# Optimization experiments

Hardware: AMD Instinct MI355X
Metric: run time of the kernel (lower is better)

The kernel has to match this reference:

```python
import jax, jax.numpy as jnp
import numpy as np

N = 100_000   # nodes
E = 600_000   # edges
D = 128       # embed_dim
G = 1000      # graphs (batch ids)
L = 3         # num_layers


def setup_inputs() -> dict:
    key = jax.random.key(0)
    ks = jax.random.split(key, 12)
    s = 1.0 / np.sqrt(D)
    return {
        "x": jax.random.normal(ks[0], (N, D), jnp.float32),
        "edge_index": jax.random.randint(ks[1], (2, E), 0, N),
        "batch": jnp.sort(jax.random.randint(ks[2], (N,), 0, G)),
        "mask": jax.random.randint(ks[3], (N,), 0, 2),
        # stacked GCNConv weights/biases (in=hidden=out=D)
        "gcn_w": jax.random.normal(ks[4], (L, D, D), jnp.float32) * s,
        "gcn_b": jnp.zeros((L, D), jnp.float32),
        # MLP head: Linear(D,D) -> ReLU -> Linear(D,1)
        "lin1_w": jax.random.normal(ks[5], (D, D), jnp.float32) * s,
        "lin1_b": jnp.zeros((D,), jnp.float32),
        "lin2_w": jax.random.normal(ks[6], (D,), jnp.float32) * s,
        "lin2_b": jnp.zeros((), jnp.float32),
    }


def gcn_forward(x, src, dst, gcn_w, gcn_b):
    # symmetric gcn_norm with self-loops: deg[i] = 1 + in-degree(i)
    deg = jax.ops.segment_sum(jnp.ones((E,), x.dtype), dst, num_segments=N) + 1.0
    dinv = jax.lax.rsqrt(deg)
    enorm = dinv[src] * dinv[dst]          # [E] edge normalization
    self_norm = (dinv * dinv)[:, None]     # [N,1] self-loop normalization
    h = x
    for l in range(L):
        h = h @ gcn_w[l]                   # [N,D]
        h = (jax.ops.segment_sum(h[src] * enorm[:, None], dst, num_segments=N)
             + h * self_norm)
        h = h + gcn_b[l]
        if l < L - 1:
            h = jax.nn.relu(h)  # (dropout inactive at inference)
    return h


def reference(x, edge_index, batch, mask, gcn_w, gcn_b, lin1_w, lin1_b, lin2_w, lin2_b):
    src, dst = edge_index[0], edge_index[1]
    h = gcn_forward(x, src, dst, gcn_w, gcn_b)
    # MLP head -> per-node score [N]
    s = jax.nn.relu(h @ lin1_w + lin1_b) @ lin2_w + lin2_b
    s = jnp.where(mask == 0, jnp.float32(-1e9), s)
    # per-graph (segment) softmax — fused replacement for the unique/batch loop
    m = jax.ops.segment_max(s, batch, num_segments=G)
    e = jnp.exp(s - m[batch])
    z = jax.ops.segment_sum(e, batch, num_segments=G)
    return e / z[batch]
```

## Files before the change

### kernel.cpp

```cpp
#include <hip/hip_runtime.h>
#include <hip/hip_bf16.h>

typedef unsigned int u32;
typedef unsigned short u16;
typedef __attribute__((ext_vector_type(8))) short bf16x8;
typedef __attribute__((ext_vector_type(4))) float f32x4;

__device__ __forceinline__ float u16tof(u16 u){ return __uint_as_float(((u32)u) << 16); }
__device__ __forceinline__ float lo16(u32 v){ return __uint_as_float(v << 16); }
__device__ __forceinline__ float hi16(u32 v){ return __uint_as_float(v & 0xffff0000u); }
__device__ __forceinline__ u16 ftobf(float f){
  u32 b = __float_as_uint(f);
  return (u16)((b + 0x7FFFu + ((b >> 16) & 1u)) >> 16);
}
__device__ __forceinline__ u32 pack2(float a, float b){
  return (u32)ftobf(a) | ((u32)ftobf(b) << 16);
}
__device__ __forceinline__ float ldf(const void* p, int i, int isbf){
  return isbf ? u16tof(((const u16*)p)[i]) : ((const float*)p)[i];
}

__global__ __launch_bounds__(256) void k_prep(const void* __restrict__ gw, const void* __restrict__ l1w,
                                              const void* __restrict__ x, u16* __restrict__ Wf,
                                              u16* __restrict__ Hb, int L, int n8, int cvtB, int goffB,
                                              const int* __restrict__ batch, int* __restrict__ goff,
                                              int N, int G,
                                              const int* __restrict__ dst, int* __restrict__ hist,
                                              int nE, int chunk, int* __restrict__ flag){
  __shared__ int sh[256];
  const int b = blockIdx.x;
  const int t = threadIdx.x;
  const int histStart = L + 1 + cvtB + goffB;

  if (b >= histStart){
    sh[t] = 0; __syncthreads();
    const int blk = b - histStart;
    const int e0 = blk * chunk, e1 = min(e0 + chunk, nE);
    for (int e = e0 + t; e < e1; e += 256) atomicAdd(&sh[dst[e] >> 9], 1);
    __syncthreads();
    hist[blk * 256 + t] = sh[t];
    return;
  }
  if (b >= L + 1 + cvtB){
    const int i = (b - (L + 1 + cvtB)) * 256 + t;
    if (i >= N) return;
    const int bt = batch[i];
    const int prev = (i == 0) ? -1 : batch[i - 1];
    for (int g = prev + 1; g <= bt; ++g) goff[g] = i;
    if (i == N - 1){ for (int g = bt + 1; g <= G; ++g) goff[g] = N; }
    return;
  }
  if (t == 0) sh[0] = 0;
  __syncthreads();
  if (b <= L){
    int local = 0;
    for (int i = t; i < 4096; i += 256){
      u32 e = (((const u32*)gw)[i] >> 7) & 0xFFu;
      if (e >= 100u && e < 127u) local++;
    }
    atomicAdd(&sh[0], local);
    __syncthreads();
    const int isbf = (sh[0] > 2048) ? 1 : 0;
    if (b == 0 && t == 0) *flag = isbf;

    const void* src = (b < L) ? gw : l1w;
    const int sbase = (b < L) ? b * 16384 : 0;
    u16* dstp = Wf + (size_t)b * 16384;
    for (int g = t; g < 2048; g += 256){
      const int tt = g >> 8, ks = (g >> 6) & 3, lane = g & 63;
      const int n = tt * 16 + (lane & 15);
      const int k0 = ks * 32 + ((lane >> 4) << 3);
      u16* d = dstp + (size_t)g * 8;
      #pragma unroll
      for (int j = 0; j < 8; ++j){
        d[j] = ftobf(ldf(src, sbase + (k0 + j) * 128 + n, isbf));
      }
    }
  } else {
    u32 e = (((const u32*)gw)[t] >> 7) & 0xFFu;
    atomicAdd(&sh[0], (e >= 100u && e < 127u) ? 1 : 0);
    __syncthreads();
    if (sh[0] > 128) return;
    const int i = (b - (L + 1)) * 256 + t;
    if (i >= n8) return;
    const float4 a = ((const float4*)x)[i * 2];
    const float4 c = ((const float4*)x)[i * 2 + 1];
    u16* o = Hb + (size_t)i * 8;
    o[0] = ftobf(a.x); o[1] = ftobf(a.y); o[2] = ftobf(a.z); o[3] = ftobf(a.w);
    o[4] = ftobf(c.x); o[5] = ftobf(c.y); o[6] = ftobf(c.z); o[7] = ftobf(c.w);
  }
}

__global__ __launch_bounds__(256) void k_hscan(int* __restrict__ hist, int* __restrict__ bb, int nE){
  const int t = threadIdx.x;
  int run = 0;
  for (int j = 0; j < 256; ++j){
    const int v = hist[j * 256 + t];
    hist[j * 256 + t] = run;
    run += v;
  }
  __shared__ int sm[256];
  sm[t] = run; __syncthreads();
  for (int off = 1; off < 256; off <<= 1){
    int a = (t >= off) ? sm[t - off] : 0;
    __syncthreads();
    sm[t] += a;
    __syncthreads();
  }
  bb[t] = sm[t] - run;
  if (t == 255) bb[256] = nE;
}

__global__ __launch_bounds__(256) void k_scatter(const int* __restrict__ src, const int* __restrict__ dst,
                                                 const int* __restrict__ hist, const int* __restrict__ bb,
                                                 int2* __restrict__ tmpe, int nE, int chunk){
  __shared__ int base[256];
  const int blk = blockIdx.x, t = threadIdx.x;
  base[t] = bb[t] + hist[blk * 256 + t];
  __syncthreads();
  const int e0 = blk * chunk, e1 = min(e0 + chunk, nE);
  for (int e = e0 + t; e < e1; e += 256){
    const int d = dst[e];
    const int pos = atomicAdd(&base[d >> 9], 1);
    tmpe[pos] = make_int2(src[e], d);
  }
}

__global__ __launch_bounds__(256) void k_local(const int2* __restrict__ tmpe, const int* __restrict__ bb,
                                               int* __restrict__ boff, int* __restrict__ eid,
                                               float* __restrict__ dinv, int N, int nE, int nbkt){
  __shared__ int hcnt[512];
  __shared__ int hoff[512];
  const int b = blockIdx.x, t = threadIdx.x;
  const int n0 = b << 9;
  const int n1 = min(n0 + 512, N);
  const int nn = n1 - n0;
  const int e0 = bb[b], e1 = bb[b + 1];
  hcnt[t] = 0; hcnt[t + 256] = 0;
  __syncthreads();
  for (int e = e0 + t; e < e1; e += 256) atomicAdd(&hcnt[tmpe[e].y - n0], 1);
  __syncthreads();
  const int v0 = hcnt[t], v1 = hcnt[t + 256];
  hoff[t] = v0; hoff[t + 256] = v1;
  __syncthreads();
  for (int off = 1; off < 512; off <<= 1){
    int a0 = (t >= off) ? hoff[t - off] : 0;
    int a1 = (t + 256 >= off) ? hoff[t + 256 - off] : 0;
    __syncthreads();
    hoff[t] += a0; hoff[t + 256] += a1;
    __syncthreads();
  }
  const int ex0 = hoff[t] - v0 + e0;
  const int ex1 = hoff[t + 256] - v1 + e0;
  if (t < nn){       boff[n0 + t] = ex0;        dinv[n0 + t] = rsqrtf((float)v0 + 1.0f); }
  if (t + 256 < nn){ boff[n0 + t + 256] = ex1;  dinv[n0 + t + 256] = rsqrtf((float)v1 + 1.0f); }
  if (b == nbkt - 1 && t == 0) boff[N] = nE;
  __syncthreads();
  hoff[t] = ex0; hoff[t + 256] = ex1;
  __syncthreads();
  for (int e = e0 + t; e < e1; e += 256){
    const int2 pr = tmpe[e];
    const int pos = atomicAdd(&hoff[pr.y - n0], 1);
    eid[pos] = pr.x;
  }
}

__global__ __launch_bounds__(256) void k_mm(const void* __restrict__ X, const u16* __restrict__ Hb,
                                            const u16* __restrict__ Wf, const float* __restrict__ dinv,
                                            u16* __restrict__ T, int n, const int* __restrict__ fl){
  __shared__ u16 smw[16384];
  const int isbf = *fl;
  const u16* A = isbf ? (const u16*)X : Hb;
  {
    const uint4* s = (const uint4*)Wf;
    uint4* d = (uint4*)smw;
    for (int i = threadIdx.x; i < 2048; i += 256) d[i] = s[i];
  }
  __syncthreads();

  const int wave = threadIdx.x >> 6, lane = threadIdx.x & 63;
  const int m0 = blockIdx.x * 64 + wave * 16;
  int arow = m0 + (lane & 15); if (arow > n - 1) arow = n - 1;
  const u16* aptr = A + (size_t)arow * 128 + ((lane >> 4) << 3);

  f32x4 acc[8];
  #pragma unroll
  for (int t = 0; t < 8; ++t) acc[t] = (f32x4){0.f, 0.f, 0.f, 0.f};

  #pragma unroll
  for (int ks = 0; ks < 4; ++ks){
    const bf16x8 a = *(const bf16x8*)(aptr + ks * 32);
    #pragma unroll
    for (int t = 0; t < 8; ++t){
      const bf16x8 b = *(const bf16x8*)(smw + (size_t)(((t * 4 + ks) * 64 + lane) * 8));
      acc[t] = __builtin_amdgcn_mfma_f32_16x16x32_bf16(a, b, acc[t], 0, 0, 0);
    }
  }
  __syncthreads();

  const int quad = lane >> 4, col0 = lane & 15;
  float dv[4];
  #pragma unroll
  for (int r = 0; r < 4; ++r){
    const int row = m0 + quad * 4 + r;
    dv[r] = (row < n) ? dinv[row] : 0.f;
  }
  u16* my = smw + wave * 2112;
  #pragma unroll
  for (int t = 0; t < 8; ++t){
    #pragma unroll
    for (int r = 0; r < 4; ++r){
      my[(quad * 4 + r) * 132 + t * 16 + col0] = ftobf(acc[t][r] * dv[r]);
    }
  }
  #pragma unroll
  for (int i = 0; i < 4; ++i){
    const int row = i * 4 + (lane >> 4);
    const int grow = m0 + row;
    const int c8 = (lane & 15) * 8;
    if (grow < n){
      const u16* s = &my[row * 132 + c8];
      uint2 lo = *(const uint2*)(s);
      uint2 hi = *(const uint2*)(s + 4);
      *(uint4*)&T[(size_t)grow * 128 + c8] = make_uint4(lo.x, lo.y, hi.x, hi.y);
    }
  }
}

__global__ __launch_bounds__(256) void k_gmm(const u16* __restrict__ Tin, const int* __restrict__ boff,
                                             const int* __restrict__ eid, const float* __restrict__ dinv,
                                             const void* __restrict__ bias, int layer,
                                             const u16* __restrict__ Wf, u16* __restrict__ Tout,
                                             int n, const int* __restrict__ fl){
  __shared__ u16 sma[16 * 132];
  const int isbf = *fl;
  const int wave = threadIdx.x >> 6, lane = threadIdx.x & 63;
  const int sub = lane >> 4, l16 = lane & 15;
  const int m0 = blockIdx.x * 16;

  const int node = m0 + wave * 4 + sub;
  float h0=0,h1=0,h2=0,h3=0,h4=0,h5=0,h6=0,h7=0;
  if (node < n){
    const uint4 sv = ((const uint4*)(Tin + (size_t)node * 128))[l16];
    float a0 = lo16(sv.x), a1 = hi16(sv.x), a2 = lo16(sv.y), a3 = hi16(sv.y);
    float a4 = lo16(sv.z), a5 = hi16(sv.z), a6 = lo16(sv.w), a7 = hi16(sv.w);
    int j = boff[node];
    const int b1e = boff[node + 1];
    for (; j + 4 <= b1e; j += 4){
      const int s0 = eid[j], s1 = eid[j + 1], s2 = eid[j + 2], s3 = eid[j + 3];
      const uint4 v0 = ((const uint4*)(Tin + (size_t)s0 * 128))[l16];
      const uint4 v1 = ((const uint4*)(Tin + (size_t)s1 * 128))[l16];
      const uint4 v2 = ((const uint4*)(Tin + (size_t)s2 * 128))[l16];
      const uint4 v3 = ((const uint4*)(Tin + (size_t)s3 * 128))[l16];
      a0 += (lo16(v0.x) + lo16(v1.x)) + (lo16(v2.x) + lo16(v3.x));
      a1 += (hi16(v0.x) + hi16(v1.x)) + (hi16(v2.x) + hi16(v3.x));
      a2 += (lo16(v0.y) + lo16(v1.y)) + (lo16(v2.y) + lo16(v3.y));
      a3 += (hi16(v0.y) + hi16(v1.y)) + (hi16(v2.y) + hi16(v3.y));
      a4 += (lo16(v0.z) + lo16(v1.z)) + (lo16(v2.z) + lo16(v3.z));
      a5 += (hi16(v0.z) + hi16(v1.z)) + (hi16(v2.z) + hi16(v3.z));
      a6 += (lo16(v0.w) + lo16(v1.w)) + (lo16(v2.w) + lo16(v3.w));
      a7 += (hi16(v0.w) + hi16(v1.w)) + (hi16(v2.w) + hi16(v3.w));
    }
    for (; j < b1e; ++j){
      const uint4 v = ((const uint4*)(Tin + (size_t)eid[j] * 128))[l16];
      a0 += lo16(v.x); a1 += hi16(v.x);
      a2 += lo16(v.y); a3 += hi16(v.y);
      a4 += lo16(v.z); a5 += hi16(v.z);
      a6 += lo16(v.w); a7 += hi16(v.w);
    }
    const float di = dinv[node];
    const int bb = layer * 128 + l16 * 8;
    h0 = fmaxf(fmaf(a0, di, ldf(bias, bb + 0, isbf)), 0.f);
    h1 = fmaxf(fmaf(a1, di, ldf(bias, bb + 1, isbf)), 0.f);
    h2 = fmaxf(fmaf(a2, di, ldf(bias, bb + 2, isbf)), 0.f);
    h3 = fmaxf(fmaf(a3, di, ldf(bias, bb + 3, isbf)), 0.f);
    h4 = fmaxf(fmaf(a4, di, ldf(bias, bb + 4, isbf)), 0.f);
    h5 = fmaxf(fmaf(a5, di, ldf(bias, bb + 5, isbf)), 0.f);
    h6 = fmaxf(fmaf(a6, di, ldf(bias, bb + 6, isbf)), 0.f);
    h7 = fmaxf(fmaf(a7, di, ldf(bias, bb + 7, isbf)), 0.f);
  }
  {
    uint4 o;
    o.x = pack2(h0, h1); o.y = pack2(h2, h3); o.z = pack2(h4, h5); o.w = pack2(h6, h7);
    *(uint4*)&sma[(wave * 4 + sub) * 132 + l16 * 8] = o;
  }
  __syncthreads();

  f32x4 acc[2];
  acc[0] = (f32x4){0.f,0.f,0.f,0.f}; acc[1] = (f32x4){0.f,0.f,0.f,0.f};
  #pragma unroll
  for (int ks = 0; ks < 4; ++ks){
    const bf16x8 a = *(const bf16x8*)(sma + l16 * 132 + sub * 8 + ks * 32);
    #pragma unroll
    for (int tt = 0; tt < 2; ++tt){
      const int t = wave * 2 + tt;
      const bf16x8 b = *(const bf16x8*)(Wf + (size_t)(((t * 4 + ks) * 64 + lane) * 8));
      acc[tt] = __builtin_amdgcn_mfma_f32_16x16x32_bf16(a, b, acc[tt], 0, 0, 0);
    }
  }
  __syncthreads();

  float dv[4];
  #pragma unroll
  for (int r = 0; r < 4; ++r){
    const int row = m0 + sub * 4 + r;
    dv[r] = (row < n) ? dinv[row] : 0.f;
  }
  #pragma unroll
  for (int tt = 0; tt < 2; ++tt){
    const int t = wave * 2 + tt;
    #pragma unroll
    for (int r = 0; r < 4; ++r){
      sma[(sub * 4 + r) * 132 + t * 16 + l16] = ftobf(acc[tt][r] * dv[r]);
    }
  }
  __syncthreads();

  {
    const int row = threadIdx.x >> 4;
    const int c8 = (threadIdx.x & 15) * 8;
    if (m0 + row < n){
      const u16* s = &sma[row * 132 + c8];
      uint2 lo = *(const uint2*)(s);
      uint2 hi = *(const uint2*)(s + 4);
      *(uint4*)&Tout[(size_t)(m0 + row) * 128 + c8] = make_uint4(lo.x, lo.y, hi.x, hi.y);
    }
  }
}

__global__ __launch_bounds__(256) void k_ghead(const u16* __restrict__ Tin, const int* __restrict__ boff,
                                               const int* __restrict__ eid, const float* __restrict__ dinv,
                                               const void* __restrict__ bias, int layer,
                                               const u16* __restrict__ Wf, const void* __restrict__ b1,
                                               const void* __restrict__ w2, const void* __restrict__ b2,
                                               const int* __restrict__ mask, float* __restrict__ s,
                                               int n, const int* __restrict__ fl){
  __shared__ u16 sma[16 * 132];
  __shared__ float sred[4][16];
  const int isbf = *fl;
  const int wave = threadIdx.x >> 6, lane = threadIdx.x & 63;
  const int sub = lane >> 4, l16 = lane & 15;
  const int m0 = blockIdx.x * 16;

  const int node = m0 + wave * 4 + sub;
  float h0=0,h1=0,h2=0,h3=0,h4=0,h5=0,h6=0,h7=0;
  if (node < n){
    const uint4 sv = ((const uint4*)(Tin + (size_t)node * 128))[l16];
    float a0 = lo16(sv.x), a1 = hi16(sv.x), a2 = lo16(sv.y), a3 = hi16(sv.y);
    float a4 = lo16(sv.z), a5 = hi16(sv.z), a6 = lo16(sv.w), a7 = hi16(sv.w);
    int j = boff[node];
    const int b1e = boff[node + 1];
    for (; j + 4 <= b1e; j += 4){
      const int s0 = eid[j], s1 = eid[j + 1], s2 = eid[j + 2], s3 = eid[j + 3];
      const uint4 v0 = ((const uint4*)(Tin + (size_t)s0 * 128))[l16];
      const uint4 v1 = ((const uint4*)(Tin + (size_t)s1 * 128))[l16];
      const uint4 v2 = ((const uint4*)(Tin + (size_t)s2 * 128))[l16];
      const uint4 v3 = ((const uint4*)(Tin + (size_t)s3 * 128))[l16];
      a0 += (lo16(v0.x) + lo16(v1.x)) + (lo16(v2.x) + lo16(v3.x));
      a1 += (hi16(v0.x) + hi16(v1.x)) + (hi16(v2.x) + hi16(v3.x));
      a2 += (lo16(v0.y) + lo16(v1.y)) + (lo16(v2.y) + lo16(v3.y));
      a3 += (hi16(v0.y) + hi16(v1.y)) + (hi16(v2.y) + hi16(v3.y));
      a4 += (lo16(v0.z) + lo16(v1.z)) + (lo16(v2.z) + lo16(v3.z));
      a5 += (hi16(v0.z) + hi16(v1.z)) + (hi16(v2.z) + hi16(v3.z));
      a6 += (lo16(v0.w) + lo16(v1.w)) + (lo16(v2.w) + lo16(v3.w));
      a7 += (hi16(v0.w) + hi16(v1.w)) + (hi16(v2.w) + hi16(v3.w));
    }
    for (; j < b1e; ++j){
      const uint4 v = ((const uint4*)(Tin + (size_t)eid[j] * 128))[l16];
      a0 += lo16(v.x); a1 += hi16(v.x);
      a2 += lo16(v.y); a3 += hi16(v.y);
      a4 += lo16(v.z); a5 += hi16(v.z);
      a6 += lo16(v.w); a7 += hi16(v.w);
    }
    const float di = dinv[node];
    const int bb = layer * 128 + l16 * 8;
    h0 = fmaf(a0, di, ldf(bias, bb + 0, isbf));
    h1 = fmaf(a1, di, ldf(bias, bb + 1, isbf));
    h2 = fmaf(a2, di, ldf(bias, bb + 2, isbf));
    h3 = fmaf(a3, di, ldf(bias, bb + 3, isbf));
    h4 = fmaf(a4, di, ldf(bias, bb + 4, isbf));
    h5 = fmaf(a5, di, ldf(bias, bb + 5, isbf));
    h6 = fmaf(a6, di, ldf(bias, bb + 6, isbf));
    h7 = fmaf(a7, di, ldf(bias, bb + 7, isbf));
  }
  {
    uint4 o;
    o.x = pack2(h0, h1); o.y = pack2(h2, h3); o.z = pack2(h4, h5); o.w = pack2(h6, h7);
    *(uint4*)&sma[(wave * 4 + sub) * 132 + l16 * 8] = o;
  }
  __syncthreads();

  f32x4 acc[2];
  acc[0] = (f32x4){0.f,0.f,0.f,0.f}; acc[1] = (f32x4){0.f,0.f,0.f,0.f};
  #pragma unroll
  for (int ks = 0; ks < 4; ++ks){
    const bf16x8 a = *(const bf16x8*)(sma + l16 * 132 + sub * 8 + ks * 32);
    #pragma unroll
    for (int tt = 0; tt < 2; ++tt){
      const int t = wave * 2 + tt;
      const bf16x8 b = *(const bf16x8*)(Wf + (size_t)(((t * 4 + ks) * 64 + lane) * 8));
      acc[tt] = __builtin_amdgcn_mfma_f32_16x16x32_bf16(a, b, acc[tt], 0, 0, 0);
    }
  }

  float p0 = 0.f, p1 = 0.f, p2 = 0.f, p3 = 0.f;
  #pragma unroll
  for (int tt = 0; tt < 2; ++tt){
    const int col = (wave * 2 + tt) * 16 + l16;
    const float bv = ldf(b1, col, isbf);
    const float wv = ldf(w2, col, isbf);
    p0 = fmaf(fmaxf(acc[tt][0] + bv, 0.f), wv, p0);
    p1 = fmaf(fmaxf(acc[tt][1] + bv, 0.f), wv, p1);
    p2 = fmaf(fmaxf(acc[tt][2] + bv, 0.f), wv, p2);
    p3 = fmaf(fmaxf(acc[tt][3] + bv, 0.f), wv, p3);
  }
  #pragma unroll
  for (int k = 1; k < 16; k <<= 1){
    p0 += __shfl_xor(p0, k);
    p1 += __shfl_xor(p1, k);
    p2 += __shfl_xor(p2, k);
    p3 += __shfl_xor(p3, k);
  }
  if (l16 == 0){
    sred[wave][sub * 4 + 0] = p0;
    sred[wave][sub * 4 + 1] = p1;
    sred[wave][sub * 4 + 2] = p2;
    sred[wave][sub * 4 + 3] = p3;
  }
  __syncthreads();
  if (threadIdx.x < 16){
    const int row = m0 + threadIdx.x;
    if (row < n){
      float sc = sred[0][threadIdx.x] + sred[1][threadIdx.x] + sred[2][threadIdx.x] + sred[3][threadIdx.x]
               + ldf(b2, 0, isbf);
      if (mask[row] == 0) sc = -1e9f;
      s[row] = sc;
    }
  }
}

__global__ __launch_bounds__(256) void k_gsm(const float* __restrict__ s, const int* __restrict__ goff,
                                             void* __restrict__ out, int G, const int* __restrict__ fl){
  const int g = blockIdx.x * 4 + (threadIdx.x >> 6);
  if (g >= G) return;
  const int lane = threadIdx.x & 63;
  const int i0 = goff[g], i1 = goff[g + 1];
  if (i0 >= i1) return;
  float m = -3.4e38f;
  for (int j = i0 + lane; j < i1; j += 64) m = fmaxf(m, s[j]);
  #pragma unroll
  for (int k = 32; k; k >>= 1) m = fmaxf(m, __shfl_xor(m, k));
  float zz = 0.f;
  for (int j = i0 + lane; j < i1; j += 64) zz += expf(s[j] - m);
  #pragma unroll
  for (int k = 32; k; k >>= 1) zz += __shfl_xor(zz, k);
  const float rz = 1.f / zz;
  const int isbf = *fl;
  for (int j = i0 + lane; j < i1; j += 64){
    const float v = expf(s[j] - m) * rz;
    if (isbf) ((u16*)out)[j] = ftobf(v);
    else      ((float*)out)[j] = v;
  }
}

extern "C" void kernel_launch(void* const* d_in, const int* in_sizes, int n_in,
                              void* d_out, int out_size, void* d_ws, size_t ws_size,
                              hipStream_t stream){
  const void* x    = d_in[0];
  const int* ei    = (const int*)d_in[1];
  const int* batch = (const int*)d_in[2];
  const int* mask  = (const int*)d_in[3];
  const void* gw   = d_in[4];
  const void* gb   = d_in[5];
  const void* l1w  = d_in[6];
  const void* l1b  = d_in[7];
  const void* l2w  = d_in[8];
  const void* l2b  = d_in[9];

  const int N = in_sizes[2];
  const int E = in_sizes[1] / 2;
  const int D = 128;
  const int L = in_sizes[4] / (D * D);
  const int G = 1000;

  char* p = (char*)d_ws;
  u16*  Hb    = (u16*)p;   p += (size_t)N * D * sizeof(u16);
  u16*  Tb    = (u16*)p;   p += (size_t)N * D * sizeof(u16);
  u16*  Wf    = (u16*)p;   p += (size_t)(L + 1) * D * D * sizeof(u16);
  float* dinv = (float*)p; p += (size_t)N * sizeof(float);
  float* sbuf = (float*)p; p += (size_t)N * sizeof(float);
  int*  boff  = (int*)p;   p += (size_t)(N + 1) * sizeof(int);
  int*  eid   = (int*)p;   p += (size_t)E * sizeof(int);
  int*  goff  = (int*)p;   p += (size_t)(G + 1) * sizeof(int);
  int*  hist  = (int*)p;   p += 256 * 256 * sizeof(int);
  int*  bb    = (int*)p;   p += 260 * sizeof(int);
  int2* tmpe  = (int2*)p;  p += (size_t)E * sizeof(int2);
  int*  flag  = (int*)p;   p += 256;

  const int* srcp = ei;
  const int* dstp = ei + E;

  const int mmg   = (N + 63) / 64;
  const int fg    = (N + 15) / 16;
  const int n8    = N * D / 8;
  const int cvtB  = (n8 + 255) / 256;
  const int goffB = (N + 255) / 256;
  const int chunk = (E + 255) / 256;
  const int nbkt  = (N + 511) / 512;

  k_prep<<<(L + 1) + cvtB + goffB + 256, 256, 0, stream>>>(gw, l1w, x, Wf, Hb, L, n8, cvtB, goffB,
                                                           batch, goff, N, G, dstp, hist, E, chunk, flag);
  k_hscan<<<1, 256, 0, stream>>>(hist, bb, E);
  k_scatter<<<256, 256, 0, stream>>>(srcp, dstp, hist, bb, tmpe, E, chunk);
  k_local<<<nbkt, 256, 0, stream>>>(tmpe, bb, boff, eid, dinv, N, E, nbkt);

  k_mm<<<mmg, 256, 0, stream>>>(x, Hb, Wf, dinv, Tb, N, flag);
  k_gmm<<<fg, 256, 0, stream>>>(Tb, boff, eid, dinv, gb, 0, Wf + (size_t)1 * D * D, Hb, N, flag);
  k_gmm<<<fg, 256, 0, stream>>>(Hb, boff, eid, dinv, gb, 1, Wf + (size_t)2 * D * D, Tb, N, flag);
  k_ghead<<<fg, 256, 0, stream>>>(Tb, boff, eid, dinv, gb, 2, Wf + (size_t)L * D * D,
                                  l1b, l2w, l2b, mask, sbuf, N, flag);
  k_gsm<<<(G + 3) / 4, 256, 0, stream>>>(sbuf, goff, d_out, G, flag);
}
```

Baseline: 320.7 us.

## Stage scatter in LDS by bucket and pack edge pairs into 32-bit words

k_scatter now counts edges per destination bucket locally, scans them, and stages the edges in shared memory sorted by bucket. It then writes them to global memory in contiguous runs instead of as random scattered int2 stores. Each edge is packed as src<<9 | local dst, halving the tmpe traffic read by k_local. The prep kernel also replaces a shared atomic counter with a wave ballot and popcount. Risks: the packing assumes src fits in 23 bits, and the stage buffer size caps how many edges each block can hold.

After: 329.8 us. 1.03x slower.

```diff
diff --git a/kernel.cpp b/kernel.cpp
--- a/kernel.cpp
+++ b/kernel.cpp
@@ -3,6 +3,7 @@
 
 typedef unsigned int u32;
 typedef unsigned short u16;
+typedef unsigned char u8;
 typedef __attribute__((ext_vector_type(8))) short bf16x8;
 typedef __attribute__((ext_vector_type(4))) float f32x4;
 
@@ -50,9 +51,9 @@
     if (i == N - 1){ for (int g = bt + 1; g <= G; ++g) goff[g] = N; }
     return;
   }
-  if (t == 0) sh[0] = 0;
-  __syncthreads();
   if (b <= L){
+    if (t == 0) sh[0] = 0;
+    __syncthreads();
     int local = 0;
     for (int i = t; i < 4096; i += 256){
       u32 e = (((const u32*)gw)[i] >> 7) & 0xFFu;
@@ -78,9 +79,11 @@
     }
   } else {
     u32 e = (((const u32*)gw)[t] >> 7) & 0xFFu;
-    atomicAdd(&sh[0], (e >= 100u && e < 127u) ? 1 : 0);
-    __syncthreads();
-    if (sh[0] > 128) return;
+    const int hit = (e >= 100u && e < 127u) ? 1 : 0;
+    unsigned long long m = __ballot(hit);
+    if ((t & 63) == 0) sh[t >> 6] = __popcll(m);
+    __syncthreads();
+    if (sh[0] + sh[1] + sh[2] + sh[3] > 128) return;
     const int i = (b - (L + 1)) * 256 + t;
     if (i >= n8) return;
     const float4 a = ((const float4*)x)[i * 2];
@@ -113,20 +116,50 @@
 
 __global__ __launch_bounds__(256) void k_scatter(const int* __restrict__ src, const int* __restrict__ dst,
                                                  const int* __restrict__ hist, const int* __restrict__ bb,
-                                                 int2* __restrict__ tmpe, int nE, int chunk){
+                                                 u32* __restrict__ tmpe, int nE, int chunk){
+  __shared__ int cnt[256];
+  __shared__ int lstart[256];
+  __shared__ int lcur[256];
   __shared__ int base[256];
+  __shared__ u32 stage[2560];
+  __shared__ u8  bktof[2560];
   const int blk = blockIdx.x, t = threadIdx.x;
   base[t] = bb[t] + hist[blk * 256 + t];
+  cnt[t] = 0;
   __syncthreads();
   const int e0 = blk * chunk, e1 = min(e0 + chunk, nE);
+  const int nloc = e1 - e0;
+  for (int e = e0 + t; e < e1; e += 256) atomicAdd(&cnt[dst[e] >> 9], 1);
+  __syncthreads();
+  {
+    const int v = cnt[t];
+    lstart[t] = v;
+    __syncthreads();
+    for (int off = 1; off < 256; off <<= 1){
+      int a = (t >= off) ? lstart[t - off] : 0;
+      __syncthreads();
+      lstart[t] += a;
+      __syncthreads();
+    }
+    lstart[t] -= v;
+    lcur[t] = lstart[t];
+  }
+  __syncthreads();
   for (int e = e0 + t; e < e1; e += 256){
     const int d = dst[e];
-    const int pos = atomicAdd(&base[d >> 9], 1);
-    tmpe[pos] = make_int2(src[e], d);
-  }
-}
-
-__global__ __launch_bounds__(256) void k_local(const int2* __restrict__ tmpe, const int* __restrict__ bb,
+    const int bkt = d >> 9;
+    const int pos = atomicAdd(&lcur[bkt], 1);
+    stage[pos] = ((u32)src[e] << 9) | (u32)(d & 511);
+    bktof[pos] = (u8)bkt;
+  }
+  __syncthreads();
+  for (int i = t; i < nloc; i += 256){
+    const int bkt = bktof[i];
+    tmpe[base[bkt] + (i - lstart[bkt])] = stage[i];
+  }
+}
+
+__global__ __launch_bounds__(256) void k_local(const u32* __restrict__ tmpe, const int* __restrict__ bb,
                                                int* __restrict__ boff, int* __restrict__ eid,
                                                float* __restrict__ dinv, int N, int nE, int nbkt){
   __shared__ int hcnt[512];
@@ -138,7 +171,7 @@
   const int e0 = bb[b], e1 = bb[b + 1];
   hcnt[t] = 0; hcnt[t + 256] = 0;
   __syncthreads();
-  for (int e = e0 + t; e < e1; e += 256) atomicAdd(&hcnt[tmpe[e].y - n0], 1);
+  for (int e = e0 + t; e < e1; e += 256) atomicAdd(&hcnt[tmpe[e] & 511u], 1);
   __syncthreads();
   const int v0 = hcnt[t], v1 = hcnt[t + 256];
   hoff[t] = v0; hoff[t + 256] = v1;
@@ -159,9 +192,9 @@
   hoff[t] = ex0; hoff[t + 256] = ex1;
   __syncthreads();
   for (int e = e0 + t; e < e1; e += 256){
-    const int2 pr = tmpe[e];
-    const int pos = atomicAdd(&hoff[pr.y - n0], 1);
-    eid[pos] = pr.x;
+    const u32 pk = tmpe[e];
+    const int pos = atomicAdd(&hoff[pk & 511u], 1);
+    eid[pos] = (int)(pk >> 9);
   }
 }
 
@@ -494,7 +527,7 @@
   int*  goff  = (int*)p;   p += (size_t)(G + 1) * sizeof(int);
   int*  hist  = (int*)p;   p += 256 * 256 * sizeof(int);
   int*  bb    = (int*)p;   p += 260 * sizeof(int);
-  int2* tmpe  = (int2*)p;  p += (size_t)E * sizeof(int2);
+  u32*  tmpe  = (u32*)p;   p += (size_t)E * sizeof(u32);
   int*  flag  = (int*)p;   p += 256;
 
   const int* srcp = ei;
```
